# Kernel tuning notes

Hardware: AMD Instinct MI355X
Metric: run time of the kernel (lower is better)

## Reference

```python
import jax, jax.numpy as jnp
import numpy as np

B, NQ, NK = 4, 2048, 2048
CQ, CK = 1024, 768
H = 16
D = CQ // H  # 64
EPS = 1e-5


def layernorm(x, gamma, beta):
    mu = jnp.mean(x, axis=-1, keepdims=True)
    var = jnp.var(x, axis=-1, keepdims=True)
    return (x - mu) * jax.lax.rsqrt(var + EPS) * gamma + beta


def setup_inputs() -> dict:
    key = jax.random.key(0)
    ks = jax.random.split(key, 12)
    s_q = 1.0 / np.sqrt(CQ)
    s_c = 1.0 / np.sqrt(CK)
    return {
        "query_tokens": jax.random.normal(ks[0], (B, NQ, CQ), jnp.float32),
        "context_tokens": jax.random.normal(ks[1], (B, NK, CK), jnp.float32),
        "Wq": jax.random.uniform(ks[2], (CQ, CQ), jnp.float32, -s_q, s_q),
        "bq": jnp.zeros((CQ,), jnp.float32),
        "Wk": jax.random.uniform(ks[3], (CK, CQ), jnp.float32, -s_c, s_c),
        "bk": jnp.zeros((CQ,), jnp.float32),
        "Wv": jax.random.uniform(ks[4], (CK, CQ), jnp.float32, -s_c, s_c),
        "bv": jnp.zeros((CQ,), jnp.float32),
        "Wo": jax.random.uniform(ks[5], (CQ, CQ), jnp.float32, -s_q, s_q),
        "bo": jnp.zeros((CQ,), jnp.float32),
        "gamma_q": jnp.ones((CQ,), jnp.float32),
        "beta_q": jnp.zeros((CQ,), jnp.float32),
        "gamma_ctx": jnp.ones((CK,), jnp.float32),
        "beta_ctx": jnp.zeros((CK,), jnp.float32),
    }


def reference(query_tokens, context_tokens, Wq, bq, Wk, bk, Wv, bv, Wo, bo,
              gamma_q, beta_q, gamma_ctx, beta_ctx):
    scale = 1.0 / np.sqrt(D)
    xq = layernorm(query_tokens, gamma_q, beta_q)      # [B,NQ,CQ]
    xc = layernorm(context_tokens, gamma_ctx, beta_ctx)  # [B,NK,CK]
    q = (xq @ Wq + bq).reshape(B, NQ, H, D)
    k = (xc @ Wk + bk).reshape(B, NK, H, D)
    v = (xc @ Wv + bv).reshape(B, NK, H, D)
    scores = jnp.einsum('bqhd,bkhd->bhqk', q, k) * scale  # [B,H,NQ,NK]
    attn = jax.nn.softmax(scores, axis=-1)
    attended = jnp.einsum('bhqk,bkhd->bqhd', attn, v).reshape(B, NQ, CQ)
    return attended @ Wo + bo
```

## Files before the change

kernel.cpp:

```cpp
#include <hip/hip_runtime.h>
#include <hip/hip_bf16.h>
#include <stdint.h>

#define B_    4
#define NQ_   2048
#define NK_   2048
#define CQ_   1024
#define CK_   768
#define H_    16
#define D_    64
#define SCALE 0.125f
#define C2    0.1803368801111204f

typedef __attribute__((ext_vector_type(8))) short bf16x8;
typedef __attribute__((ext_vector_type(4))) float f32x4;
typedef __attribute__((ext_vector_type(4))) unsigned int u32x4;

#define MFMA16(a, b, c) __builtin_amdgcn_mfma_f32_16x16x32_bf16((a), (b), (c), 0, 0, 0)

#define GLL16(gp, lp)                                                                 \
    __builtin_amdgcn_global_load_lds(                                                 \
        (__attribute__((address_space(1))) uint32_t*)(uintptr_t)(gp),                 \
        (__attribute__((address_space(3))) uint32_t*)(uintptr_t)(lp), 16, 0, 0)

__device__ inline unsigned short f2bf(float f) {
    union { float f; uint32_t u; } v; v.f = f;
    uint32_t u = v.u;
    return (unsigned short)((u + 0x7fffu + ((u >> 16) & 1u)) >> 16);
}

__device__ inline uint32_t packbf2(float a, float b) {
    union { __hip_bfloat162 h; uint32_t u; } v;
    v.h = __float22bfloat162_rn(float2{a, b});
    return v.u;
}

__global__ __launch_bounds__(256) void ln_tr(const float* __restrict__ xqt,
                                             const float* __restrict__ xct,
                                             const float* __restrict__ gq,
                                             const float* __restrict__ btq,
                                             const float* __restrict__ gc,
                                             const float* __restrict__ btc,
                                             unsigned short* __restrict__ oq,
                                             unsigned short* __restrict__ oc,
                                             const float* __restrict__ Wq,
                                             const float* __restrict__ Wk,
                                             const float* __restrict__ Wv,
                                             const float* __restrict__ Wo,
                                             unsigned short* __restrict__ Wqt,
                                             unsigned short* __restrict__ Wkvt,
                                             unsigned short* __restrict__ Wot) {
    __shared__ float red[8];
    __shared__ float stat[2];
    __shared__ float tt[32][33];
    int blk = blockIdx.x;
    int tid = threadIdx.x;

    if (blk < 16384) {
        const float *x, *gamma, *beta;
        unsigned short* out;
        int W;
        float invW;
        if (blk < 8192) {
            x = xqt + (size_t)blk * 1024; gamma = gq; beta = btq;
            out = oq + (size_t)blk * 1024; W = 1024; invW = 1.f / 1024.f;
        } else {
            int r = blk - 8192;
            x = xct + (size_t)r * 768; gamma = gc; beta = btc;
            out = oc + (size_t)r * 768; W = 768; invW = 1.f / 768.f;
        }
        int col = tid * 4;
        float v0 = 0.f, v1 = 0.f, v2 = 0.f, v3 = 0.f;
        float s = 0.f, s2 = 0.f;
        bool active = (col < W);
        if (active) {
            float4 vv = *(const float4*)(x + col);
            v0 = vv.x; v1 = vv.y; v2 = vv.z; v3 = vv.w;
            s = v0 + v1 + v2 + v3;
            s2 = v0 * v0 + v1 * v1 + v2 * v2 + v3 * v3;
        }
        for (int off = 32; off >= 1; off >>= 1) {
            s += __shfl_xor(s, off);
            s2 += __shfl_xor(s2, off);
        }
        int wid = tid >> 6, lane = tid & 63;
        if (lane == 0) { red[wid] = s; red[4 + wid] = s2; }
        __syncthreads();
        if (tid == 0) {
            float ts = red[0] + red[1] + red[2] + red[3];
            float ts2 = red[4] + red[5] + red[6] + red[7];
            float mu = ts * invW;
            float var = ts2 * invW - mu * mu;
            stat[0] = mu;
            stat[1] = rsqrtf(var + 1e-5f);
        }
        __syncthreads();
        float mu = stat[0], rstd = stat[1];
        if (active) {
            float4 gm = *(const float4*)(gamma + col);
            float4 bt = *(const float4*)(beta + col);
            ushort4 o;
            o.x = f2bf((v0 - mu) * rstd * gm.x + bt.x);
            o.y = f2bf((v1 - mu) * rstd * gm.y + bt.y);
            o.z = f2bf((v2 - mu) * rstd * gm.z + bt.z);
            o.w = f2bf((v3 - mu) * rstd * gm.w + bt.w);
            *(ushort4*)(out + col) = o;
        }
    } else {
        int b2 = blk - 16384;
        const float* src;
        unsigned short* dst;
        int K;
        if (b2 < 1024)      { src = Wq; dst = Wqt; K = 1024; }
        else if (b2 < 1792) { b2 -= 1024; src = Wk; dst = Wkvt; K = 768; }
        else if (b2 < 2560) { b2 -= 1792; src = Wv; dst = Wkvt + (size_t)1024 * 768; K = 768; }
        else                 { b2 -= 2560; src = Wo; dst = Wot; K = 1024; }
        int n0 = (b2 & 31) * 32, k0 = (b2 >> 5) * 32;
        int tx = tid & 31, ty = tid >> 5;
        for (int i = 0; i < 4; i++)
            tt[ty + 8 * i][tx] = src[(size_t)(k0 + ty + 8 * i) * 1024 + n0 + tx];
        __syncthreads();
        for (int i = 0; i < 4; i++)
            dst[(size_t)(n0 + ty + 8 * i) * K + k0 + tx] = f2bf(tt[tx][ty + 8 * i]);
    }
}

__global__ __launch_bounds__(256) void gemm_qkv(const unsigned short* __restrict__ xq,
                                                const unsigned short* __restrict__ Wqt,
                                                const float* __restrict__ bq,
                                                const unsigned short* __restrict__ xc,
                                                const unsigned short* __restrict__ Wkvt,
                                                const float* __restrict__ bk,
                                                const float* __restrict__ bv,
                                                unsigned short* __restrict__ Qb,
                                                unsigned short* __restrict__ Kb,
                                                unsigned short* __restrict__ Vtb) {
    __shared__ __align__(16) unsigned short As[128 * 64];
    __shared__ __align__(16) unsigned short Bs[128 * 64];
    int tid = threadIdx.x;
    int lane = tid & 63, wid = tid >> 6;

    int lin = blockIdx.x;
    int xcd = lin & 7;
    int idx = lin >> 3;
    const unsigned short *X, *Wt;
    int Kd, NB, sub, qrole;
    if (idx < 64) { X = xq; Wt = Wqt;  Kd = 1024; NB = 8;  sub = xcd * 64 + idx;          qrole = 1; }
    else          { X = xc; Wt = Wkvt; Kd = 768;  NB = 16; sub = xcd * 128 + (idx - 64);  qrole = 0; }
    int m0 = (sub / NB) * 128;
    int n0 = (sub % NB) * 128;
    int wm = wid >> 1, wn = wid & 1;

    f32x4 acc[4][4];
    for (int i = 0; i < 4; i++)
        for (int j = 0; j < 4; j++) acc[i][j] = (f32x4){0.f, 0.f, 0.f, 0.f};

    int srow = wid * 8 + (lane >> 3);
    int sxor = ((lane & 7) * 16) ^ (((lane >> 3) & 7) << 4);
    int swz = (lane & 7) << 4;
    const char* Xb = (const char*)X;
    const char* Wb = (const char*)Wt;
    char* AsB = (char*)As;
    char* BsB = (char*)Bs;

    for (int k0 = 0; k0 < Kd; k0 += 64) {
        for (int i = 0; i < 4; i++) {
            int row = i * 32 + srow;
            GLL16(Xb + ((size_t)(m0 + row) * Kd + k0) * 2 + sxor, AsB + i * 4096 + wid * 1024);
            GLL16(Wb + ((size_t)(n0 + row) * Kd + k0) * 2 + sxor, BsB + i * 4096 + wid * 1024);
        }
        __syncthreads();
        for (int kk = 0; kk < 2; kk++) {
            int cb = (((lane >> 4) * 16 + kk * 64) ^ swz);
            bf16x8 a[4], b[4];
            for (int mf = 0; mf < 4; mf++)
                a[mf] = *(const bf16x8*)(AsB + (wm * 64 + mf * 16 + (lane & 15)) * 128 + cb);
            for (int nf = 0; nf < 4; nf++)
                b[nf] = *(const bf16x8*)(BsB + (wn * 64 + nf * 16 + (lane & 15)) * 128 + cb);
            for (int mf = 0; mf < 4; mf++)
                for (int nf = 0; nf < 4; nf++) acc[mf][nf] = MFMA16(a[mf], b[nf], acc[mf][nf]);
        }
        __syncthreads();
    }

    int crow0 = m0 + wm * 64;
    int ccol0 = n0 + wn * 64;
    for (int nf = 0; nf < 4; nf++) {
        int col = ccol0 + nf * 16 + (lane & 15);
        float bv_ = qrole ? bq[col] : ((col < 1024) ? bk[col] : bv[col - 1024]);
        if (!qrole && col >= 1024) {
            int c = col - 1024;
            int h = c >> 6, d = c & 63;
            for (int mf = 0; mf < 4; mf++) {
                int rowb = crow0 + mf * 16 + (lane >> 4) * 4;
                int b = rowb >> 11;
                int nqb = rowb & 2047;
                int u = nqb & 63;
                int pbase = (nqb & ~63) | ((u & 32) + ((u & 12) << 1) + ((u & 16) >> 2));
                ushort4 o;
                o.x = f2bf(acc[mf][nf][0] + bv_);
                o.y = f2bf(acc[mf][nf][1] + bv_);
                o.z = f2bf(acc[mf][nf][2] + bv_);
                o.w = f2bf(acc[mf][nf][3] + bv_);
                *(ushort4*)&Vtb[(((size_t)(b * H_ + h)) * 64 + d) * NK_ + pbase] = o;
            }
        } else {
            for (int mf = 0; mf < 4; mf++) {
                int rowb = crow0 + mf * 16 + (lane >> 4) * 4;
                for (int r = 0; r < 4; r++) {
                    int row = rowb + r;
                    float val = acc[mf][nf][r] + bv_;
                    int b = row >> 11, nq = row & 2047;
                    int h = col >> 6, d = col & 63;
                    if (qrole) {
                        Qb[(((size_t)(b * H_ + h)) * NQ_ + nq) * 64 + d] = f2bf(val * C2);
                    } else {
                        Kb[(((size_t)(b * H_ + h)) * NQ_ + nq) * 64 + d] = f2bf(val);
                    }
                }
            }
        }
    }
}

__global__ __launch_bounds__(256) void gemm_out(const unsigned short* __restrict__ X,
                                                const unsigned short* __restrict__ Wt,
                                                const float* __restrict__ bias0,
                                                float* __restrict__ out0) {
    __shared__ __align__(16) unsigned short As[128 * 64];
    __shared__ __align__(16) unsigned short Bs[128 * 64];
    int tid = threadIdx.x;
    int lane = tid & 63, wid = tid >> 6;
    const int Kd = 1024;

    int lin = blockIdx.y * 8 + blockIdx.x;
    int virt = (lin & 7) * 64 + (lin >> 3);
    int m0 = (virt / 8) * 128;
    int n0 = (virt % 8) * 128;
    int wm = wid >> 1, wn = wid & 1;

    f32x4 acc[4][4];
    for (int i = 0; i < 4; i++)
        for (int j = 0; j < 4; j++) acc[i][j] = (f32x4){0.f, 0.f, 0.f, 0.f};

    int srow = wid * 8 + (lane >> 3);
    int sxor = ((lane & 7) * 16) ^ (((lane >> 3) & 7) << 4);
    int swz = (lane & 7) << 4;
    const char* Xb = (const char*)X;
    const char* Wb = (const char*)Wt;
    char* AsB = (char*)As;
    char* BsB = (char*)Bs;

    for (int k0 = 0; k0 < Kd; k0 += 64) {
        for (int i = 0; i < 4; i++) {
            int row = i * 32 + srow;
            GLL16(Xb + ((size_t)(m0 + row) * Kd + k0) * 2 + sxor, AsB + i * 4096 + wid * 1024);
            GLL16(Wb + ((size_t)(n0 + row) * Kd + k0) * 2 + sxor, BsB + i * 4096 + wid * 1024);
        }
        __syncthreads();
        for (int kk = 0; kk < 2; kk++) {
            int cb = (((lane >> 4) * 16 + kk * 64) ^ swz);
            bf16x8 a[4], b[4];
            for (int mf = 0; mf < 4; mf++)
                a[mf] = *(const bf16x8*)(AsB + (wm * 64 + mf * 16 + (lane & 15)) * 128 + cb);
            for (int nf = 0; nf < 4; nf++)
                b[nf] = *(const bf16x8*)(BsB + (wn * 64 + nf * 16 + (lane & 15)) * 128 + cb);
            for (int mf = 0; mf < 4; mf++)
                for (int nf = 0; nf < 4; nf++) acc[mf][nf] = MFMA16(a[mf], b[nf], acc[mf][nf]);
        }
        __syncthreads();
    }

    int crow0 = m0 + wm * 64;
    int ccol0 = n0 + wn * 64;
    for (int nf = 0; nf < 4; nf++) {
        int col = ccol0 + nf * 16 + (lane & 15);
        float bv_ = bias0[col];
        for (int mf = 0; mf < 4; mf++) {
            int rowb = crow0 + mf * 16 + (lane >> 4) * 4;
            for (int r = 0; r < 4; r++) {
                int row = rowb + r;
                out0[(size_t)row * 1024 + col] = acc[mf][nf][r] + bv_;
            }
        }
    }
}

__global__ __launch_bounds__(512, 4) void flash_attn(const unsigned short* __restrict__ Q,
                                                     const unsigned short* __restrict__ K,
                                                     const unsigned short* __restrict__ Vt,
                                                     unsigned short* __restrict__ attended) {
    __shared__ __align__(16) char smem[4][16384];
    int tid = threadIdx.x, lane = tid & 63, wid = tid >> 6;
    int g = lane >> 4;
    int q = lane & 15;

    const f32x4 zero4 = {0.f, 0.f, 0.f, 0.f};

    int lin = blockIdx.y * 8 + blockIdx.x;
    int virt = (lin & 7) * 64 + (lin >> 3);
    int bh = virt >> 3;
    int q0 = (virt & 7) * 256;
    const char* Qb = (const char*)(Q + (size_t)bh * NQ_ * 64);
    const char* Kb = (const char*)(K + (size_t)bh * NK_ * 64);
    const char* Vb = (const char*)(Vt + (size_t)bh * 64 * NK_);

    int qrow = q0 + wid * 32 + q;
    bf16x8 qf0[2], qf1[2];
    qf0[0] = *(const bf16x8*)(Qb + (size_t)qrow * 128 + g * 16);
    qf0[1] = *(const bf16x8*)(Qb + (size_t)qrow * 128 + g * 16 + 64);
    qf1[0] = *(const bf16x8*)(Qb + (size_t)(qrow + 16) * 128 + g * 16);
    qf1[1] = *(const bf16x8*)(Qb + (size_t)(qrow + 16) * 128 + g * 16 + 64);

    bf16x8 onesf;
#pragma unroll
    for (int i = 0; i < 8; i++) onesf[i] = (short)0x3f80;

    f32x4 acc0[4], acc1[4];
    for (int i = 0; i < 4; i++) {
        acc0[i] = zero4;
        acc1[i] = zero4;
    }
    f32x4 accl0 = zero4, accl1 = zero4;

    int sxor = ((lane & 7) * 16) ^ (((lane >> 3) & 7) << 4);
    const char* kptr = Kb + (size_t)(wid * 8 + (lane >> 3)) * 128 + sxor;
    const char* vptr = Vb + (size_t)(wid * 8 + (lane >> 3)) * 4096 + sxor;
    int cb0 = g * 16;
    int swz = (lane & 7) << 4;

    auto TILE = [&](const char* Ksb, const char* Vsb) {
        f32x4 s0[4], s1[4];
        __builtin_amdgcn_s_setprio(1);
#pragma unroll
        for (int nf = 0; nf < 4; nf++) {
            bf16x8 kf0 = *(const bf16x8*)(Ksb + (nf * 16 + q) * 128 + (cb0 ^ swz));
            bf16x8 kf1 = *(const bf16x8*)(Ksb + (nf * 16 + q) * 128 + ((cb0 + 64) ^ swz));
            s0[nf] = MFMA16(kf0, qf0[0], zero4);
            s0[nf] = MFMA16(kf1, qf0[1], s0[nf]);
            s1[nf] = MFMA16(kf0, qf1[0], zero4);
            s1[nf] = MFMA16(kf1, qf1[1], s1[nf]);
        }
        __builtin_amdgcn_s_setprio(0);

        __builtin_amdgcn_s_setprio(1);
#pragma unroll
        for (int kk = 0; kk < 2; kk++) {
            float p0v[8], p1v[8];
#pragma unroll
            for (int h = 0; h < 2; h++)
#pragma unroll
                for (int r = 0; r < 4; r++) {
                    p0v[4 * h + r] = __builtin_amdgcn_exp2f(s0[2 * kk + h][r]);
                    p1v[4 * h + r] = __builtin_amdgcn_exp2f(s1[2 * kk + h][r]);
                }
            union { u32x4 u; bf16x8 b; } ap0, ap1;
            ap0.u[0] = packbf2(p0v[0], p0v[1]);
            ap0.u[1] = packbf2(p0v[2], p0v[3]);
            ap0.u[2] = packbf2(p0v[4], p0v[5]);
            ap0.u[3] = packbf2(p0v[6], p0v[7]);
            ap1.u[0] = packbf2(p1v[0], p1v[1]);
            ap1.u[1] = packbf2(p1v[2], p1v[3]);
            ap1.u[2] = packbf2(p1v[4], p1v[5]);
            ap1.u[3] = packbf2(p1v[6], p1v[7]);

            accl0 = MFMA16(ap0.b, onesf, accl0);
            accl1 = MFMA16(ap1.b, onesf, accl1);
#pragma unroll
            for (int df = 0; df < 4; df++) {
                bf16x8 bv = *(const bf16x8*)(Vsb + (df * 16 + q) * 128 + ((cb0 + kk * 64) ^ swz));
                acc0[df] = MFMA16(ap0.b, bv, acc0[df]);
                acc1[df] = MFMA16(ap1.b, bv, acc1[df]);
            }
        }
        __builtin_amdgcn_s_setprio(0);
    };

#pragma unroll
    for (int j = 0; j < 4; j++) {
        GLL16(kptr, smem[j] + wid * 1024);
        GLL16(vptr, smem[j] + 8192 + wid * 1024);
        kptr += 8192;
        vptr += 128;
    }
    __syncthreads();

    for (int i = 0; i < 16; ++i) {
        int t = 2 * i;
        const char* B0 = smem[t & 3];
        const char* B1 = smem[(t + 1) & 3];
        TILE(B0, B0 + 8192);
        TILE(B1, B1 + 8192);
        __syncthreads();
        if (t + 4 < 32) {
            GLL16(kptr, smem[t & 3] + wid * 1024);
            GLL16(vptr, smem[t & 3] + 8192 + wid * 1024);
            kptr += 8192;
            vptr += 128;
            GLL16(kptr, smem[(t + 1) & 3] + wid * 1024);
            GLL16(vptr, smem[(t + 1) & 3] + 8192 + wid * 1024);
            kptr += 8192;
            vptr += 128;
        }
    }

    int b = bh >> 4, h = bh & 15;
#pragma unroll
    for (int df = 0; df < 4; df++)
#pragma unroll
        for (int r = 0; r < 4; r++) {
            int row = q0 + wid * 32 + 4 * g + r;
            int col = h * 64 + df * 16 + q;
            attended[(size_t)(b * NQ_ + row) * CQ_ + col] = f2bf(acc0[df][r] / accl0[r]);
            attended[(size_t)(b * NQ_ + row + 16) * CQ_ + col] = f2bf(acc1[df][r] / accl1[r]);
        }
}

extern "C" void kernel_launch(void* const* d_in, const int* in_sizes, int n_in,
                              void* d_out, int out_size, void* d_ws, size_t ws_size,
                              hipStream_t stream) {
    const float* qt  = (const float*)d_in[0];
    const float* ct  = (const float*)d_in[1];
    const float* Wq  = (const float*)d_in[2];
    const float* bq  = (const float*)d_in[3];
    const float* Wk  = (const float*)d_in[4];
    const float* bk  = (const float*)d_in[5];
    const float* Wv  = (const float*)d_in[6];
    const float* bv  = (const float*)d_in[7];
    const float* Wo  = (const float*)d_in[8];
    const float* bo  = (const float*)d_in[9];
    const float* gq  = (const float*)d_in[10];
    const float* btq = (const float*)d_in[11];
    const float* gc  = (const float*)d_in[12];
    const float* btc = (const float*)d_in[13];

    char* ws = (char*)d_ws;
    unsigned short* xq   = (unsigned short*)(ws + 0);
    unsigned short* xc   = (unsigned short*)(ws + 16777216);
    unsigned short* Wqt  = (unsigned short*)(ws + 29360128);
    unsigned short* Wkvt = (unsigned short*)(ws + 31457280);
    unsigned short* Wot  = (unsigned short*)(ws + 34603008);
    unsigned short* Qb   = (unsigned short*)(ws + 36700160);
    unsigned short* Kb   = (unsigned short*)(ws + 53477376);
    unsigned short* Vtb  = (unsigned short*)(ws + 70254592);

    ln_tr<<<19968, 256, 0, stream>>>(qt, ct, gq, btq, gc, btc, xq, xc,
                                     Wq, Wk, Wv, Wo, Wqt, Wkvt, Wot);

    gemm_qkv<<<1536, 256, 0, stream>>>(xq, Wqt, bq, xc, Wkvt, bk, bv, Qb, Kb, Vtb);

    flash_attn<<<dim3(8, 64), 512, 0, stream>>>(Qb, Kb, Vtb, xq);

    gemm_out<<<dim3(8, 64), 256, 0, stream>>>(xq, Wot, bo, (float*)d_out);
}
```

Before: 177.9 us.

## Pipeline GEMM K-loop with four-stage LDS ring of 32-wide K tiles

Both projection GEMMs now split K into 32-wide tiles held in a 4-buffer LDS ring. Four tiles are prefetched via global_load_lds, and two are consumed per barrier while the next two are issued. This overlaps global loads with MFMA work and halves the number of barriers compared with the old load-sync-compute-sync loop. The LDS swizzle is adapted to the 64-byte row layout. Total LDS per block stays 32 KB, but the correctness of the ring's buffer reuse depends on the barrier placement and on how the loads are waited on.

```diff
diff --git a/kernel.cpp b/kernel.cpp
--- a/kernel.cpp
+++ b/kernel.cpp
@@ -135,10 +135,11 @@
                                                 unsigned short* __restrict__ Qb,
                                                 unsigned short* __restrict__ Kb,
                                                 unsigned short* __restrict__ Vtb) {
-    __shared__ __align__(16) unsigned short As[128 * 64];
-    __shared__ __align__(16) unsigned short Bs[128 * 64];
+    __shared__ __align__(16) unsigned short As[4][128 * 32];
+    __shared__ __align__(16) unsigned short Bs[4][128 * 32];
     int tid = threadIdx.x;
     int lane = tid & 63, wid = tid >> 6;
+    int q = lane & 15, g = lane >> 4;
 
     int lin = blockIdx.x;
     int xcd = lin & 7;
@@ -155,44 +156,67 @@
     for (int i = 0; i < 4; i++)
         for (int j = 0; j < 4; j++) acc[i][j] = (f32x4){0.f, 0.f, 0.f, 0.f};
 
-    int srow = wid * 8 + (lane >> 3);
-    int sxor = ((lane & 7) * 16) ^ (((lane >> 3) & 7) << 4);
-    int swz = (lane & 7) << 4;
+    int sx2 = (((lane & 3) ^ ((lane >> 2) & 3)) << 4);
+    int srow0 = wid * 32 + (lane >> 2);
     const char* Xb = (const char*)X;
     const char* Wb = (const char*)Wt;
     char* AsB = (char*)As;
     char* BsB = (char*)Bs;
 
-    for (int k0 = 0; k0 < Kd; k0 += 64) {
-        for (int i = 0; i < 4; i++) {
-            int row = i * 32 + srow;
-            GLL16(Xb + ((size_t)(m0 + row) * Kd + k0) * 2 + sxor, AsB + i * 4096 + wid * 1024);
-            GLL16(Wb + ((size_t)(n0 + row) * Kd + k0) * 2 + sxor, BsB + i * 4096 + wid * 1024);
-        }
+    auto STAGE = [&](int buf, int t) {
+#pragma unroll
+        for (int c = 0; c < 2; c++) {
+            int row = srow0 + c * 16;
+            GLL16(Xb + ((size_t)(m0 + row) * Kd + t * 32) * 2 + sx2,
+                  AsB + buf * 8192 + wid * 2048 + c * 1024);
+            GLL16(Wb + ((size_t)(n0 + row) * Kd + t * 32) * 2 + sx2,
+                  BsB + buf * 8192 + wid * 2048 + c * 1024);
+        }
+    };
+
+    int ck = (g ^ (q & 3)) << 4;
+    auto COMPUTE = [&](int buf) {
+        bf16x8 a[4], b[4];
+#pragma unroll
+        for (int mf = 0; mf < 4; mf++)
+            a[mf] = *(const bf16x8*)(AsB + buf * 8192 + (wm * 64 + mf * 16 + q) * 64 + ck);
+#pragma unroll
+        for (int nf = 0; nf < 4; nf++)
+            b[nf] = *(const bf16x8*)(BsB + buf * 8192 + (wn * 64 + nf * 16 + q) * 64 + ck);
+#pragma unroll
+        for (int mf = 0; mf < 4; mf++)
+#pragma unroll
+            for (int nf = 0; nf < 4; nf++) acc[mf][nf] = MFMA16(a[mf], b[nf], acc[mf][nf]);
+    };
+
+    int nT = Kd >> 5;
+    STAGE(0, 0);
+    STAGE(1, 1);
+    STAGE(2, 2);
+    STAGE(3, 3);
+    __syncthreads();
+
+    for (int i = 0; i < nT / 2; i++) {
+        int t = 2 * i;
+        COMPUTE(t & 3);
+        COMPUTE((t + 1) & 3);
         __syncthreads();
-        for (int kk = 0; kk < 2; kk++) {
-            int cb = (((lane >> 4) * 16 + kk * 64) ^ swz);
-            bf16x8 a[4], b[4];
-            for (int mf = 0; mf < 4; mf++)
-                a[mf] = *(const bf16x8*)(AsB + (wm * 64 + mf * 16 + (lane & 15)) * 128 + cb);
-            for (int nf = 0; nf < 4; nf++)
-                b[nf] = *(const bf16x8*)(BsB + (wn * 64 + nf * 16 + (lane & 15)) * 128 + cb);
-            for (int mf = 0; mf < 4; mf++)
-                for (int nf = 0; nf < 4; nf++) acc[mf][nf] = MFMA16(a[mf], b[nf], acc[mf][nf]);
-        }
-        __syncthreads();
+        if (t + 4 < nT) {
+            STAGE(t & 3, t + 4);
+            STAGE((t + 1) & 3, t + 5);
+        }
     }
 
     int crow0 = m0 + wm * 64;
     int ccol0 = n0 + wn * 64;
     for (int nf = 0; nf < 4; nf++) {
-        int col = ccol0 + nf * 16 + (lane & 15);
+        int col = ccol0 + nf * 16 + q;
         float bv_ = qrole ? bq[col] : ((col < 1024) ? bk[col] : bv[col - 1024]);
         if (!qrole && col >= 1024) {
             int c = col - 1024;
             int h = c >> 6, d = c & 63;
             for (int mf = 0; mf < 4; mf++) {
-                int rowb = crow0 + mf * 16 + (lane >> 4) * 4;
+                int rowb = crow0 + mf * 16 + g * 4;
                 int b = rowb >> 11;
                 int nqb = rowb & 2047;
                 int u = nqb & 63;
@@ -206,7 +230,7 @@
             }
         } else {
             for (int mf = 0; mf < 4; mf++) {
-                int rowb = crow0 + mf * 16 + (lane >> 4) * 4;
+                int rowb = crow0 + mf * 16 + g * 4;
                 for (int r = 0; r < 4; r++) {
                     int row = rowb + r;
                     float val = acc[mf][nf][r] + bv_;
@@ -227,10 +251,11 @@
                                                 const unsigned short* __restrict__ Wt,
                                                 const float* __restrict__ bias0,
                                                 float* __restrict__ out0) {
-    __shared__ __align__(16) unsigned short As[128 * 64];
-    __shared__ __align__(16) unsigned short Bs[128 * 64];
+    __shared__ __align__(16) unsigned short As[4][128 * 32];
+    __shared__ __align__(16) unsigned short Bs[4][128 * 32];
     int tid = threadIdx.x;
     int lane = tid & 63, wid = tid >> 6;
+    int q = lane & 15, g = lane >> 4;
     const int Kd = 1024;
 
     int lin = blockIdx.y * 8 + blockIdx.x;
@@ -243,41 +268,64 @@
     for (int i = 0; i < 4; i++)
         for (int j = 0; j < 4; j++) acc[i][j] = (f32x4){0.f, 0.f, 0.f, 0.f};
 
-    int srow = wid * 8 + (lane >> 3);
-    int sxor = ((lane & 7) * 16) ^ (((lane >> 3) & 7) << 4);
-    int swz = (lane & 7) << 4;
+    int sx2 = (((lane & 3) ^ ((lane >> 2) & 3)) << 4);
+    int srow0 = wid * 32 + (lane >> 2);
     const char* Xb = (const char*)X;
     const char* Wb = (const char*)Wt;
     char* AsB = (char*)As;
     char* BsB = (char*)Bs;
 
-    for (int k0 = 0; k0 < Kd; k0 += 64) {
-        for (int i = 0; i < 4; i++) {
-            int row = i * 32 + srow;
-            GLL16(Xb + ((size_t)(m0 + row) * Kd + k0) * 2 + sxor, AsB + i * 4096 + wid * 1024);
-            GLL16(Wb + ((size_t)(n0 + row) * Kd + k0) * 2 + sxor, BsB + i * 4096 + wid * 1024);
-        }
+    auto STAGE = [&](int buf, int t) {
+#pragma unroll
+        for (int c = 0; c < 2; c++) {
+            int row = srow0 + c * 16;
+            GLL16(Xb + ((size_t)(m0 + row) * Kd + t * 32) * 2 + sx2,
+                  AsB + buf * 8192 + wid * 2048 + c * 1024);
+            GLL16(Wb + ((size_t)(n0 + row) * Kd + t * 32) * 2 + sx2,
+                  BsB + buf * 8192 + wid * 2048 + c * 1024);
+        }
+    };
+
+    int ck = (g ^ (q & 3)) << 4;
+    auto COMPUTE = [&](int buf) {
+        bf16x8 a[4], b[4];
+#pragma unroll
+        for (int mf = 0; mf < 4; mf++)
+            a[mf] = *(const bf16x8*)(AsB + buf * 8192 + (wm * 64 + mf * 16 + q) * 64 + ck);
+#pragma unroll
+        for (int nf = 0; nf < 4; nf++)
+            b[nf] = *(const bf16x8*)(BsB + buf * 8192 + (wn * 64 + nf * 16 + q) * 64 + ck);
+#pragma unroll
+        for (int mf = 0; mf < 4; mf++)
+#pragma unroll
+            for (int nf = 0; nf < 4; nf++) acc[mf][nf] = MFMA16(a[mf], b[nf], acc[mf][nf]);
+    };
+
+    const int nT = 32;
+    STAGE(0, 0);
+    STAGE(1, 1);
+    STAGE(2, 2);
+    STAGE(3, 3);
+    __syncthreads();
+
+    for (int i = 0; i < nT / 2; i++) {
+        int t = 2 * i;
+        COMPUTE(t & 3);
+        COMPUTE((t + 1) & 3);
         __syncthreads();
-        for (int kk = 0; kk < 2; kk++) {
-            int cb = (((lane >> 4) * 16 + kk * 64) ^ swz);
-            bf16x8 a[4], b[4];
-            for (int mf = 0; mf < 4; mf++)
-                a[mf] = *(const bf16x8*)(AsB + (wm * 64 + mf * 16 + (lane & 15)) * 128 + cb);
-            for (int nf = 0; nf < 4; nf++)
-                b[nf] = *(const bf16x8*)(BsB + (wn * 64 + nf * 16 + (lane & 15)) * 128 + cb);
-            for (int mf = 0; mf < 4; mf++)
-                for (int nf = 0; nf < 4; nf++) acc[mf][nf] = MFMA16(a[mf], b[nf], acc[mf][nf]);
-        }
-        __syncthreads();
+        if (t + 4 < nT) {
+            STAGE(t & 3, t + 4);
+            STAGE((t + 1) & 3, t + 5);
+        }
     }
 
     int crow0 = m0 + wm * 64;
     int ccol0 = n0 + wn * 64;
     for (int nf = 0; nf < 4; nf++) {
-        int col = ccol0 + nf * 16 + (lane & 15);
+        int col = ccol0 + nf * 16 + q;
         float bv_ = bias0[col];
         for (int mf = 0; mf < 4; mf++) {
-            int rowb = crow0 + mf * 16 + (lane >> 4) * 4;
+            int rowb = crow0 + mf * 16 + g * 4;
             for (int r = 0; r < 4; r++) {
                 int row = rowb + r;
                 out0[(size_t)row * 1024 + col] = acc[mf][nf][r] + bv_;
```

Measured after the change: 177.1 us. No clear change (-0.4%).
